# Kernel optimization log

Measured on AMD Instinct MI355X. Metric: run time of the kernel, lower is better.

Reference implementation:

```python
import jax, jax.numpy as jnp
import numpy as np

C = 768
H = 12
T = 4096
B = 1
EPS = 1e-5


def setup_inputs() -> dict:
    key = jax.random.key(0)
    ks = jax.random.split(key, 16)
    s = 0.02
    return {
        "x": jax.random.normal(ks[0], (B, T, C), jnp.float32),
        "ln1_w": jnp.ones((C,), jnp.float32),
        "ln1_b": jnp.zeros((C,), jnp.float32),
        "W_attn": jax.random.normal(ks[1], (C, 3 * C), jnp.float32) * s,
        "b_attn": jnp.zeros((3 * C,), jnp.float32),
        "W_proj": jax.random.normal(ks[2], (C, C), jnp.float32) * s,
        "b_proj": jnp.zeros((C,), jnp.float32),
        "ln2_w": jnp.ones((C,), jnp.float32),
        "ln2_b": jnp.zeros((C,), jnp.float32),
        "W_fc": jax.random.normal(ks[3], (C, 4 * C), jnp.float32) * s,
        "b_fc": jnp.zeros((4 * C,), jnp.float32),
        "W_fc2": jax.random.normal(ks[4], (4 * C, C), jnp.float32) * s,
        "b_fc2": jnp.zeros((C,), jnp.float32),
    }


def _layernorm(x, w, b):
    mu = jnp.mean(x, axis=-1, keepdims=True)
    var = jnp.var(x, axis=-1, keepdims=True)
    return (x - mu) * jax.lax.rsqrt(var + EPS) * w + b


def _attn(x, W_attn, b_attn, W_proj, b_proj):
    Bb, Tt, Cc = x.shape
    hd = Cc // H
    qkv = x @ W_attn + b_attn                       # (B,T,3C)
    q, k, v = jnp.split(qkv, 3, axis=-1)
    q = q.reshape(Bb, Tt, H, hd).transpose(0, 2, 1, 3)  # (B,H,T,hd)
    k = k.reshape(Bb, Tt, H, hd).transpose(0, 2, 1, 3)
    v = v.reshape(Bb, Tt, H, hd).transpose(0, 2, 1, 3)
    att = jnp.einsum('bhqd,bhkd->bhqk', q, k) * (1.0 / np.sqrt(hd))
    causal = jnp.tril(jnp.ones((Tt, Tt), bool))
    att = jnp.where(causal, att, -jnp.inf)
    att = jax.nn.softmax(att, axis=-1)
    y = jnp.einsum('bhqk,bhkd->bhqd', att, v)       # (B,H,T,hd)
    y = y.transpose(0, 2, 1, 3).reshape(Bb, Tt, Cc)
    return y @ W_proj + b_proj


def _mlp(x, W_fc, b_fc, W_fc2, b_fc2):
    h = jax.nn.gelu(x @ W_fc + b_fc, approximate=False)
    return h @ W_fc2 + b_fc2


def reference(x, ln1_w, ln1_b, W_attn, b_attn, W_proj, b_proj,
              ln2_w, ln2_b, W_fc, b_fc, W_fc2, b_fc2):
    x = x + _attn(_layernorm(x, ln1_w, ln1_b), W_attn, b_attn, W_proj, b_proj)
    x = x + _mlp(_layernorm(x, ln2_w, ln2_b), W_fc, b_fc, W_fc2, b_fc2)
    return x
```

## Files before the change

kernel.cpp:

```cpp
#include <hip/hip_runtime.h>
#include <hip/hip_bf16.h>
#include <math.h>

#define TSEQ 4096
#define CDIM 768
#define NH 12
#define HD 64

typedef float f32x4 __attribute__((ext_vector_type(4)));
typedef __bf16 bf16x8 __attribute__((ext_vector_type(8)));
typedef short s16x8 __attribute__((ext_vector_type(8)));
typedef uint u32x4 __attribute__((ext_vector_type(4)));

__device__ inline ushort f2bf(float f) {
  __hip_bfloat16 h = __float2bfloat16(f);
  return __builtin_bit_cast(ushort, h);
}

__device__ inline void async16(const void* g, void* l) {
  __builtin_amdgcn_global_load_lds(
      (__attribute__((address_space(1))) unsigned int*)(uintptr_t)g,
      (__attribute__((address_space(3))) unsigned int*)(uintptr_t)l, 16, 0, 0);
}

__device__ inline void barrier_all() {
  asm volatile("s_waitcnt vmcnt(0) lgkmcnt(0)" ::: "memory");
  __builtin_amdgcn_sched_barrier(0);
  __builtin_amdgcn_s_barrier();
  __builtin_amdgcn_sched_barrier(0);
}

__device__ inline float exp2_fast(float x) {
  float r;
  asm volatile("v_exp_f32 %0, %1\n\ts_nop 0" : "=v"(r) : "v"(x));
  return r;
}

__device__ inline uint cvtpk(float a, float b) {
  uint r;
  asm volatile("v_cvt_pk_bf16_f32 %0, %1, %2" : "=v"(r) : "v"(a), "v"(b));
  return r;
}

__device__ inline bf16x8 frag_read(const ushort* base, int row, int kk, int lane) {
  const int byte = row * 128 + ((((kk * 4 + (lane >> 4)) ^ (row & 7))) << 4);
  return *(const bf16x8*)((const char*)base + byte);
}

__global__ __launch_bounds__(256) void wconv_t(
    const float* __restrict__ W, ushort* __restrict__ Wt, int K, int N)
{
  __shared__ float sm[32][33];
  const int n0 = blockIdx.x * 32, k0 = blockIdx.y * 32;
  const int c = threadIdx.x & 31, r0 = threadIdx.x >> 5;
#pragma unroll
  for (int i = 0; i < 4; ++i) {
    const int r = r0 + i * 8;
    sm[r][c] = W[(size_t)(k0 + r) * N + n0 + c];
  }
  __syncthreads();
#pragma unroll
  for (int i = 0; i < 4; ++i) {
    const int r = r0 + i * 8;
    Wt[(size_t)(n0 + r) * K + k0 + c] = f2bf(sm[c][r]);
  }
}

__global__ __launch_bounds__(256) void ln_kernel(
    const float* __restrict__ x, const float* __restrict__ w,
    const float* __restrict__ b, ushort* __restrict__ out)
{
  const int row = blockIdx.x;
  const int tid = threadIdx.x;
  const float* xr = x + (size_t)row * CDIM;
  float v[3];
  float s1 = 0.f, s2 = 0.f;
#pragma unroll
  for (int i = 0; i < 3; ++i) {
    v[i] = xr[tid + i * 256];
    s1 += v[i];
    s2 += v[i] * v[i];
  }
#pragma unroll
  for (int off = 32; off >= 1; off >>= 1) {
    s1 += __shfl_xor(s1, off, 64);
    s2 += __shfl_xor(s2, off, 64);
  }
  __shared__ float red1[4], red2[4];
  if ((tid & 63) == 0) { red1[tid >> 6] = s1; red2[tid >> 6] = s2; }
  __syncthreads();
  s1 = red1[0] + red1[1] + red1[2] + red1[3];
  s2 = red2[0] + red2[1] + red2[2] + red2[3];
  const float mu = s1 * (1.f / CDIM);
  const float var = s2 * (1.f / CDIM) - mu * mu;
  const float inv = rsqrtf(var + 1e-5f);
#pragma unroll
  for (int i = 0; i < 3; ++i) {
    const int c = tid + i * 256;
    out[(size_t)row * CDIM + c] = f2bf((v[i] - mu) * inv * w[c] + b[c]);
  }
}

template <int EPI, int BN>
__global__ __launch_bounds__(256) void gemm_bt(
    const ushort* __restrict__ A, const ushort* __restrict__ Bt,
    const float* __restrict__ bias, const float* __restrict__ res,
    ushort* __restrict__ outb, float* __restrict__ outf,
    int M, int N, int K, int gx)
{
  constexpr int NW = BN / 32;
  __shared__ __align__(16) ushort As[2][128 * 32];
  __shared__ __align__(16) ushort Bs[2][BN * 32];
  const int tid = threadIdx.x;
  const int lane = tid & 63;
  const int wv = tid >> 6;
  const int nwg = (int)gridDim.x;
  const int bid = (int)blockIdx.x;
  const int sw = (bid & 7) * (nwg >> 3) + (bid >> 3);
  const int rowBase = (sw / gx) * 128;
  const int colBase = (sw % gx) * BN;
  const int wr = (wv >> 1) * 64;
  const int wc = (wv & 1) * (BN / 2);

  f32x4 acc[4][NW] = {};

  const int e0 = tid * 8;
  const int r0 = e0 >> 5, c0 = e0 & 31;
  const int e1 = (tid + 256) * 8;
  const int r1 = e1 >> 5, c1 = e1 & 31;

  const ushort* Ag0 = A + (size_t)(rowBase + r0) * K + c0;
  const ushort* Ag1 = A + (size_t)(rowBase + r1) * K + c1;
  const ushort* Bg0 = Bt + (size_t)(colBase + r0) * K + c0;
  const ushort* Bg1 = Bt + (size_t)(colBase + r1) * K + c1;

  auto stage = [&](int buf, int k0) {
    async16(Ag0 + k0, &As[buf][e0]);
    async16(Ag1 + k0, &As[buf][e1]);
    async16(Bg0 + k0, &Bs[buf][e0]);
    if (BN == 128) async16(Bg1 + k0, &Bs[buf][e1]);
  };

  stage(0, 0);
  int buf = 0;
  for (int k0 = 0; k0 < K; k0 += 32) {
    barrier_all();
    if (k0 + 32 < K) stage(buf ^ 1, k0 + 32);
    bf16x8 af[4], bfr[NW];
#pragma unroll
    for (int m = 0; m < 4; ++m)
      af[m] = *(const bf16x8*)&As[buf][(wr + m * 16 + (lane & 15)) * 32 + (lane >> 4) * 8];
#pragma unroll
    for (int n = 0; n < NW; ++n)
      bfr[n] = *(const bf16x8*)&Bs[buf][(wc + n * 16 + (lane & 15)) * 32 + (lane >> 4) * 8];
#pragma unroll
    for (int m = 0; m < 4; ++m)
#pragma unroll
      for (int n = 0; n < NW; ++n)
        acc[m][n] = __builtin_amdgcn_mfma_f32_16x16x32_bf16(af[m], bfr[n], acc[m][n], 0, 0, 0);
    buf ^= 1;
  }

#pragma unroll
  for (int n = 0; n < NW; ++n) {
    const int gc = colBase + wc + n * 16 + (lane & 15);
    const float bv = bias[gc];
#pragma unroll
    for (int m = 0; m < 4; ++m) {
#pragma unroll
      for (int j = 0; j < 4; ++j) {
        const int gr = rowBase + wr + m * 16 + (lane >> 4) * 4 + j;
        const float v = acc[m][n][j] + bv;
        if (EPI == 0) {
          outb[(size_t)gr * N + gc] = f2bf(v);
        } else if (EPI == 1) {
          outf[(size_t)gr * N + gc] = res[(size_t)gr * N + gc] + v;
        } else {
          const float g = 0.5f * v * (1.0f + erff(v * 0.70710678118654752f));
          outb[(size_t)gr * N + gc] = f2bf(g);
        }
      }
    }
  }
}

__global__ __launch_bounds__(256) void attn_kernel(
    const ushort* __restrict__ qkv, ushort* __restrict__ att)
{
  __shared__ __align__(16) ushort Ks[2][64 * 64];
  __shared__ __align__(16) ushort Vt[2][64 * 64];

  const int tid = threadIdx.x;
  const int lane = tid & 63;
  const int wv = tid >> 6;
  const int g = lane >> 4;
  const int ql = lane & 15;
  const int p_ = blockIdx.x & 255, grp = blockIdx.x >> 8;
  const int item = (grp & 1) ? (grp * 256 + 255 - p_) : (grp * 256 + p_);
  const int qb = 63 - (item / 12);
  const int h = item % 12;
  const int t0 = qb * 64;
  const size_t rs = 3 * CDIM;
  const int qo = h * HD, ko = CDIM + h * HD, vo = 2 * CDIM + h * HD;

  const float cexp = 0.18033688f;
  const float cbias = -32.0f * 0.18033688f;

  const int L0 = tid * 16, L1 = (tid + 256) * 16;
  const int r_0 = L0 >> 7, c_0 = ((L0 >> 4) & 7) ^ (r_0 & 7);
  const int r_1 = L1 >> 7, c_1 = ((L1 >> 4) & 7) ^ (r_1 & 7);
  const ushort* kg0 = qkv + (size_t)r_0 * rs + ko + c_0 * 8;
  const ushort* kg1 = qkv + (size_t)r_1 * rs + ko + c_1 * 8;

  const int vt = (tid >> 3) * 2;
  const int vd = (tid & 7) * 8;
  const int slot2 = (32 * ((vt >> 4) >> 1) + 8 * ((vt >> 2) & 3) +
                     4 * ((vt >> 4) & 1) + (vt & 3)) * 2;
  const ushort* vg = qkv + (size_t)vt * rs + vo + vd;

  const ushort* qrow = qkv + (size_t)(t0 + wv * 16 + ql) * rs + qo + g * 8;
  const bf16x8 aq0 = *(const bf16x8*)(qrow);
  const bf16x8 aq1 = *(const bf16x8*)(qrow + 32);

  s16x8 vA0 = *(const s16x8*)(vg);
  s16x8 vA1 = *(const s16x8*)(vg + rs);
  async16(kg0, (char*)Ks[0] + L0);
  async16(kg1, (char*)Ks[0] + L1);
  asm volatile("s_waitcnt vmcnt(0)" ::: "memory");
#pragma unroll
  for (int jj = 0; jj < 8; ++jj) {
    const int d = vd + jj;
    const uint val = (uint)(ushort)vA0[jj] | ((uint)(ushort)vA1[jj] << 16);
    *(uint*)((char*)Vt[0] + d * 128 + (slot2 ^ (((d >> 1) & 7) << 4))) = val;
  }

  float lsum = 0.f;
  f32x4 accO[4] = {};
  const int swzv = (ql >> 1) & 7;

  auto body = [&](int kb, int cur, bool diag) {
    barrier_all();

    s16x8 vN0, vN1;
    const bool pre = (kb < qb);
    if (pre) {
      const size_t koff = (size_t)(kb + 1) * 64 * rs;
      vN0 = *(const s16x8*)(vg + koff);
      vN1 = *(const s16x8*)(vg + koff + rs);
      async16(kg0 + koff, (char*)Ks[cur ^ 1] + L0);
      async16(kg1 + koff, (char*)Ks[cur ^ 1] + L1);
    }

    f32x4 accS[4] = {};
    __builtin_amdgcn_s_setprio(1);
#pragma unroll
    for (int kk = 0; kk < 2; ++kk) {
      const bf16x8 a_q = kk ? aq1 : aq0;
#pragma unroll
      for (int n = 0; n < 4; ++n)
        accS[n] = __builtin_amdgcn_mfma_f32_16x16x32_bf16(
            frag_read(Ks[cur], n * 16 + ql, kk, lane), a_q, accS[n], 0, 0, 0);
    }
    __builtin_amdgcn_s_setprio(0);

    uint pk[8];
#pragma unroll
    for (int n = 0; n < 4; ++n) {
      float pv[4];
#pragma unroll
      for (int j = 0; j < 4; ++j) {
        float s = exp2_fast(fmaf(accS[n][j], cexp, cbias));
        if (diag && (kb * 64 + 16 * n + 4 * g + j) > (t0 + wv * 16 + ql)) s = 0.f;
        pv[j] = s;
        lsum += s;
      }
      pk[2 * n] = cvtpk(pv[0], pv[1]);
      pk[2 * n + 1] = cvtpk(pv[2], pv[3]);
    }
    const bf16x8 pf0 = __builtin_bit_cast(bf16x8, (u32x4){pk[0], pk[1], pk[2], pk[3]});
    const bf16x8 pf1 = __builtin_bit_cast(bf16x8, (u32x4){pk[4], pk[5], pk[6], pk[7]});

    __builtin_amdgcn_s_setprio(1);
#pragma unroll
    for (int kk = 0; kk < 2; ++kk) {
      const bf16x8 a_p = kk ? pf1 : pf0;
#pragma unroll
      for (int n = 0; n < 4; ++n) {
        const int byte = (n * 16 + ql) * 128 + ((kk * 64 + g * 16) ^ (swzv << 4));
        const bf16x8 bv = *(const bf16x8*)((const char*)Vt[cur] + byte);
        accO[n] = __builtin_amdgcn_mfma_f32_16x16x32_bf16(a_p, bv, accO[n], 0, 0, 0);
      }
    }
    __builtin_amdgcn_s_setprio(0);

    if (pre) {
#pragma unroll
      for (int jj = 0; jj < 8; ++jj) {
        const int d = vd + jj;
        const uint val = (uint)(ushort)vN0[jj] | ((uint)(ushort)vN1[jj] << 16);
        *(uint*)((char*)Vt[cur ^ 1] + d * 128 + (slot2 ^ (((d >> 1) & 7) << 4))) = val;
      }
    }
  };

  int cur = 0;
  for (int kb = 0; kb < qb; ++kb) {
    body(kb, cur, false);
    cur ^= 1;
  }
  body(qb, cur, true);

  lsum += __shfl_xor(lsum, 16, 64);
  lsum += __shfl_xor(lsum, 32, 64);
  float inv[4];
#pragma unroll
  for (int jr = 0; jr < 4; ++jr)
    inv[jr] = 1.0f / __shfl(lsum, 4 * g + jr, 64);
#pragma unroll
  for (int n = 0; n < 4; ++n)
#pragma unroll
    for (int jr = 0; jr < 4; ++jr) {
      const int tq = t0 + wv * 16 + 4 * g + jr;
      const int d = n * 16 + ql;
      att[(size_t)tq * CDIM + h * HD + d] = f2bf(accO[n][jr] * inv[jr]);
    }
}

extern "C" void kernel_launch(void* const* d_in, const int* in_sizes, int n_in,
                              void* d_out, int out_size, void* d_ws, size_t ws_size,
                              hipStream_t stream)
{
  const float* x      = (const float*)d_in[0];
  const float* ln1_w  = (const float*)d_in[1];
  const float* ln1_b  = (const float*)d_in[2];
  const float* W_attn = (const float*)d_in[3];
  const float* b_attn = (const float*)d_in[4];
  const float* W_proj = (const float*)d_in[5];
  const float* b_proj = (const float*)d_in[6];
  const float* ln2_w  = (const float*)d_in[7];
  const float* ln2_b  = (const float*)d_in[8];
  const float* W_fc   = (const float*)d_in[9];
  const float* b_fc   = (const float*)d_in[10];
  const float* W_fc2  = (const float*)d_in[11];
  const float* b_fc2  = (const float*)d_in[12];
  float* out = (float*)d_out;

  char* base = (char*)d_ws;
  size_t off = 0;
  auto alloc = [&](size_t bytes) -> void* {
    void* q = base + off;
    off = (off + bytes + 255) & ~(size_t)255;
    return q;
  };
  ushort* Wt_attn = (ushort*)alloc(768ull * 2304 * 2);
  ushort* Wt_proj = (ushort*)alloc(768ull * 768 * 2);
  ushort* Wt_fc   = (ushort*)alloc(768ull * 3072 * 2);
  ushort* Wt_fc2  = (ushort*)alloc(3072ull * 768 * 2);
  ushort* t_ln    = (ushort*)alloc(4096ull * 768 * 2);
  ushort* t_att   = (ushort*)alloc(4096ull * 768 * 2);
  float*  t_x1    = (float*) alloc(4096ull * 768 * 4);
  ushort* t_big   = (ushort*)alloc(4096ull * 3072 * 2);
  ushort* t_qkv = t_big;
  ushort* t_h   = t_big;

  wconv_t<<<dim3(2304 / 32, 768 / 32), 256, 0, stream>>>(W_attn, Wt_attn, 768, 2304);
  wconv_t<<<dim3(768 / 32, 768 / 32), 256, 0, stream>>>(W_proj, Wt_proj, 768, 768);
  wconv_t<<<dim3(3072 / 32, 768 / 32), 256, 0, stream>>>(W_fc, Wt_fc, 768, 3072);
  wconv_t<<<dim3(768 / 32, 3072 / 32), 256, 0, stream>>>(W_fc2, Wt_fc2, 3072, 768);

  ln_kernel<<<4096, 256, 0, stream>>>(x, ln1_w, ln1_b, t_ln);
  gemm_bt<0, 128><<<18 * 32, 256, 0, stream>>>(
      t_ln, Wt_attn, b_attn, nullptr, t_qkv, nullptr, 4096, 2304, 768, 18);
  attn_kernel<<<dim3(768), 256, 0, stream>>>(t_qkv, t_att);
  gemm_bt<1, 64><<<12 * 32, 256, 0, stream>>>(
      t_att, Wt_proj, b_proj, x, nullptr, t_x1, 4096, 768, 768, 12);
  ln_kernel<<<4096, 256, 0, stream>>>(t_x1, ln2_w, ln2_b, t_ln);
  gemm_bt<2, 128><<<24 * 32, 256, 0, stream>>>(
      t_ln, Wt_fc, b_fc, nullptr, t_h, nullptr, 4096, 3072, 768, 24);
  gemm_bt<1, 64><<<12 * 32, 256, 0, stream>>>(
      t_h, Wt_fc2, b_fc2, t_x1, nullptr, out, 4096, 768, 3072, 12);
}
```

Measured before the change: 202.2 us.

## Split attention KV range across waves with per-wave staging and LDS reduction

Restructures the attention kernel so each of the four waves handles all 64 queries of the block but a strided quarter of the key/value blocks, using its own private K/V LDS buffers. Inter-wave barriers disappear from the main loop, and each K/V fragment read from LDS is reused across four query groups. The row sum is computed with an MFMA against a vector of ones instead of scalar adds, and the partial outputs are combined through a 96KB LDS reduction at the end. In exchange it uses far more LDS and registers (launch bounds force one block per SM slot), adds an epilogue reduction, and can leave waves unevenly loaded on short causal rows.

```diff
diff --git a/kernel.cpp b/kernel.cpp
--- a/kernel.cpp
+++ b/kernel.cpp
@@ -184,146 +184,189 @@
   }
 }
 
-__global__ __launch_bounds__(256) void attn_kernel(
+__global__ __launch_bounds__(256, 1) void attn_kernel(
     const ushort* __restrict__ qkv, ushort* __restrict__ att)
 {
-  __shared__ __align__(16) ushort Ks[2][64 * 64];
-  __shared__ __align__(16) ushort Vt[2][64 * 64];
-
+  __shared__ __align__(16) char smem[98304];
   const int tid = threadIdx.x;
   const int lane = tid & 63;
   const int wv = tid >> 6;
-  const int g = lane >> 4;
+  const int g = (lane >> 4) & 3;
   const int ql = lane & 15;
   const int p_ = blockIdx.x & 255, grp = blockIdx.x >> 8;
   const int item = (grp & 1) ? (grp * 256 + 255 - p_) : (grp * 256 + p_);
-  const int qb = 63 - (item / 12);
+  const int qb = 63 - item / 12;
   const int h = item % 12;
   const int t0 = qb * 64;
-  const size_t rs = 3 * CDIM;
+  const int rs = 3 * CDIM;
   const int qo = h * HD, ko = CDIM + h * HD, vo = 2 * CDIM + h * HD;
 
   const float cexp = 0.18033688f;
   const float cbias = -32.0f * 0.18033688f;
 
-  const int L0 = tid * 16, L1 = (tid + 256) * 16;
-  const int r_0 = L0 >> 7, c_0 = ((L0 >> 4) & 7) ^ (r_0 & 7);
-  const int r_1 = L1 >> 7, c_1 = ((L1 >> 4) & 7) ^ (r_1 & 7);
-  const ushort* kg0 = qkv + (size_t)r_0 * rs + ko + c_0 * 8;
-  const ushort* kg1 = qkv + (size_t)r_1 * rs + ko + c_1 * 8;
-
-  const int vt = (tid >> 3) * 2;
-  const int vd = (tid & 7) * 8;
-  const int slot2 = (32 * ((vt >> 4) >> 1) + 8 * ((vt >> 2) & 3) +
-                     4 * ((vt >> 4) & 1) + (vt & 3)) * 2;
-  const ushort* vg = qkv + (size_t)vt * rs + vo + vd;
-
-  const ushort* qrow = qkv + (size_t)(t0 + wv * 16 + ql) * rs + qo + g * 8;
-  const bf16x8 aq0 = *(const bf16x8*)(qrow);
-  const bf16x8 aq1 = *(const bf16x8*)(qrow + 32);
-
-  s16x8 vA0 = *(const s16x8*)(vg);
-  s16x8 vA1 = *(const s16x8*)(vg + rs);
-  async16(kg0, (char*)Ks[0] + L0);
-  async16(kg1, (char*)Ks[0] + L1);
-  asm volatile("s_waitcnt vmcnt(0)" ::: "memory");
-#pragma unroll
-  for (int jj = 0; jj < 8; ++jj) {
-    const int d = vd + jj;
-    const uint val = (uint)(ushort)vA0[jj] | ((uint)(ushort)vA1[jj] << 16);
-    *(uint*)((char*)Vt[0] + d * 128 + (slot2 ^ (((d >> 1) & 7) << 4))) = val;
-  }
-
-  float lsum = 0.f;
-  f32x4 accO[4] = {};
-  const int swzv = (ql >> 1) & 7;
-
-  auto body = [&](int kb, int cur, bool diag) {
-    barrier_all();
-
-    s16x8 vN0, vN1;
-    const bool pre = (kb < qb);
-    if (pre) {
-      const size_t koff = (size_t)(kb + 1) * 64 * rs;
-      vN0 = *(const s16x8*)(vg + koff);
-      vN1 = *(const s16x8*)(vg + koff + rs);
-      async16(kg0 + koff, (char*)Ks[cur ^ 1] + L0);
-      async16(kg1 + koff, (char*)Ks[cur ^ 1] + L1);
-    }
-
-    f32x4 accS[4] = {};
-    __builtin_amdgcn_s_setprio(1);
-#pragma unroll
-    for (int kk = 0; kk < 2; ++kk) {
-      const bf16x8 a_q = kk ? aq1 : aq0;
-#pragma unroll
-      for (int n = 0; n < 4; ++n)
-        accS[n] = __builtin_amdgcn_mfma_f32_16x16x32_bf16(
-            frag_read(Ks[cur], n * 16 + ql, kk, lane), a_q, accS[n], 0, 0, 0);
-    }
-    __builtin_amdgcn_s_setprio(0);
-
-    uint pk[8];
-#pragma unroll
-    for (int n = 0; n < 4; ++n) {
-      float pv[4];
-#pragma unroll
-      for (int j = 0; j < 4; ++j) {
-        float s = exp2_fast(fmaf(accS[n][j], cexp, cbias));
-        if (diag && (kb * 64 + 16 * n + 4 * g + j) > (t0 + wv * 16 + ql)) s = 0.f;
-        pv[j] = s;
-        lsum += s;
-      }
-      pk[2 * n] = cvtpk(pv[0], pv[1]);
-      pk[2 * n + 1] = cvtpk(pv[2], pv[3]);
-    }
-    const bf16x8 pf0 = __builtin_bit_cast(bf16x8, (u32x4){pk[0], pk[1], pk[2], pk[3]});
-    const bf16x8 pf1 = __builtin_bit_cast(bf16x8, (u32x4){pk[4], pk[5], pk[6], pk[7]});
-
-    __builtin_amdgcn_s_setprio(1);
-#pragma unroll
-    for (int kk = 0; kk < 2; ++kk) {
-      const bf16x8 a_p = kk ? pf1 : pf0;
-#pragma unroll
-      for (int n = 0; n < 4; ++n) {
-        const int byte = (n * 16 + ql) * 128 + ((kk * 64 + g * 16) ^ (swzv << 4));
-        const bf16x8 bv = *(const bf16x8*)((const char*)Vt[cur] + byte);
-        accO[n] = __builtin_amdgcn_mfma_f32_16x16x32_bf16(a_p, bv, accO[n], 0, 0, 0);
-      }
-    }
-    __builtin_amdgcn_s_setprio(0);
-
-    if (pre) {
+  char* wbase = smem + wv * 24576;
+  char* vtile = wbase + 16384;
+
+  bf16x8 qf[4][2];
+#pragma unroll
+  for (int qg = 0; qg < 4; ++qg) {
+    const ushort* qrow = qkv + (size_t)(t0 + 16 * qg + ql) * rs + qo + g * 8;
+    qf[qg][0] = *(const bf16x8*)(qrow);
+    qf[qg][1] = *(const bf16x8*)(qrow + 32);
+  }
+
+  const int krow = lane >> 3;
+  const ushort* bKsrc = qkv + (size_t)(wv * 64 + krow) * rs + ko + ((lane & 7) ^ krow) * 8;
+
+  const int vt2 = (lane >> 3) * 2;
+  const int vd = (lane & 7) * 8;
+  const ushort* bVsrc = qkv + (size_t)(wv * 64 + vt2) * rs + vo + vd;
+  int slot2[4];
+#pragma unroll
+  for (int i = 0; i < 4; ++i)
+    slot2[i] = (32 * (i >> 1) + 8 * (vt2 >> 2) + 4 * (i & 1) + (vt2 & 3)) * 2;
+
+  const int nt = (qb >= wv) ? ((qb - wv) >> 2) + 1 : 0;
+
+  auto stageK = [&](int buf, size_t koff) {
+    char* dK = wbase + buf * 8192;
+#pragma unroll
+    for (int i = 0; i < 8; ++i)
+      async16(bKsrc + koff + (size_t)i * 8 * rs, dK + i * 1024 + lane * 16);
+  };
+
+  s16x8 vr[4][2];
+  if (nt > 0) {
+    stageK(0, 0);
+#pragma unroll
+    for (int i = 0; i < 4; ++i) {
+      vr[i][0] = *(const s16x8*)(bVsrc + (size_t)i * 16 * rs);
+      vr[i][1] = *(const s16x8*)(bVsrc + (size_t)i * 16 * rs + rs);
+    }
+  }
+
+  f32x4 accO[4][4] = {};
+  f32x4 accL[4] = {};
+  const bf16x8 ones = __builtin_bit_cast(bf16x8,
+      (u32x4){0x3F803F80u, 0x3F803F80u, 0x3F803F80u, 0x3F803F80u});
+
+  int kv0 = wv * 64;
+  int cur = 0;
+  for (int it = 0; it < nt; ++it) {
+    asm volatile("s_waitcnt vmcnt(0)" ::: "memory");
+    __builtin_amdgcn_sched_barrier(0);
+    const size_t nextoff = (size_t)(it + 1) * 256 * rs;
+    const bool pre = (it + 1 < nt);
+    if (pre) stageK(cur ^ 1, nextoff);
+
+#pragma unroll
+    for (int i = 0; i < 4; ++i) {
 #pragma unroll
       for (int jj = 0; jj < 8; ++jj) {
         const int d = vd + jj;
-        const uint val = (uint)(ushort)vN0[jj] | ((uint)(ushort)vN1[jj] << 16);
-        *(uint*)((char*)Vt[cur ^ 1] + d * 128 + (slot2 ^ (((d >> 1) & 7) << 4))) = val;
-      }
-    }
-  };
-
-  int cur = 0;
-  for (int kb = 0; kb < qb; ++kb) {
-    body(kb, cur, false);
+        const uint val = (uint)(ushort)vr[i][0][jj] | ((uint)(ushort)vr[i][1][jj] << 16);
+        *(uint*)(vtile + d * 128 + (slot2[i] ^ (((d >> 1) & 7) << 4))) = val;
+      }
+    }
+    if (pre) {
+#pragma unroll
+      for (int i = 0; i < 4; ++i) {
+        vr[i][0] = *(const s16x8*)(bVsrc + nextoff + (size_t)i * 16 * rs);
+        vr[i][1] = *(const s16x8*)(bVsrc + nextoff + (size_t)i * 16 * rs + rs);
+      }
+    }
+
+    const ushort* Kt = (const ushort*)(wbase + cur * 8192);
+    const bool diag = (kv0 == t0);
+    uint paw[4][8];
+#pragma unroll
+    for (int kg = 0; kg < 4; ++kg) {
+      const bf16x8 A0 = frag_read(Kt, kg * 16 + ql, 0, lane);
+      const bf16x8 A1 = frag_read(Kt, kg * 16 + ql, 1, lane);
+      f32x4 s[4];
+#pragma unroll
+      for (int qg = 0; qg < 4; ++qg) {
+        s[qg] = __builtin_amdgcn_mfma_f32_16x16x32_bf16(A0, qf[qg][0], (f32x4){0.f, 0.f, 0.f, 0.f}, 0, 0, 0);
+        s[qg] = __builtin_amdgcn_mfma_f32_16x16x32_bf16(A1, qf[qg][1], s[qg], 0, 0, 0);
+      }
+#pragma unroll
+      for (int qg = 0; qg < 4; ++qg) {
+        float e[4];
+#pragma unroll
+        for (int j = 0; j < 4; ++j) {
+          float p = exp2_fast(fmaf(s[qg][j], cexp, cbias));
+          if (diag && (kv0 + kg * 16 + 4 * g + j) > (t0 + 16 * qg + ql)) p = 0.f;
+          e[j] = p;
+        }
+        paw[qg][(kg >> 1) * 4 + (kg & 1) * 2]     = cvtpk(e[0], e[1]);
+        paw[qg][(kg >> 1) * 4 + (kg & 1) * 2 + 1] = cvtpk(e[2], e[3]);
+      }
+    }
+    bf16x8 pa[4][2];
+#pragma unroll
+    for (int qg = 0; qg < 4; ++qg) {
+      pa[qg][0] = __builtin_bit_cast(bf16x8, (u32x4){paw[qg][0], paw[qg][1], paw[qg][2], paw[qg][3]});
+      pa[qg][1] = __builtin_bit_cast(bf16x8, (u32x4){paw[qg][4], paw[qg][5], paw[qg][6], paw[qg][7]});
+    }
+
+    asm volatile("s_waitcnt lgkmcnt(0)" ::: "memory");
+    __builtin_amdgcn_sched_barrier(0);
+
+#pragma unroll
+    for (int dg = 0; dg < 4; ++dg) {
+#pragma unroll
+      for (int kk = 0; kk < 2; ++kk) {
+        const int byte = (16 * dg + ql) * 128 + ((kk * 64 + g * 16) ^ (((ql >> 1) & 7) << 4));
+        const bf16x8 bv = *(const bf16x8*)(vtile + byte);
+#pragma unroll
+        for (int qg = 0; qg < 4; ++qg)
+          accO[qg][dg] = __builtin_amdgcn_mfma_f32_16x16x32_bf16(pa[qg][kk], bv, accO[qg][dg], 0, 0, 0);
+      }
+    }
+#pragma unroll
+    for (int qg = 0; qg < 4; ++qg) {
+      accL[qg] = __builtin_amdgcn_mfma_f32_16x16x32_bf16(pa[qg][0], ones, accL[qg], 0, 0, 0);
+      accL[qg] = __builtin_amdgcn_mfma_f32_16x16x32_bf16(pa[qg][1], ones, accL[qg], 0, 0, 0);
+    }
+    kv0 += 256;
     cur ^= 1;
   }
-  body(qb, cur, true);
-
-  lsum += __shfl_xor(lsum, 16, 64);
-  lsum += __shfl_xor(lsum, 32, 64);
-  float inv[4];
-#pragma unroll
-  for (int jr = 0; jr < 4; ++jr)
-    inv[jr] = 1.0f / __shfl(lsum, 4 * g + jr, 64);
-#pragma unroll
-  for (int n = 0; n < 4; ++n)
-#pragma unroll
-    for (int jr = 0; jr < 4; ++jr) {
-      const int tq = t0 + wv * 16 + 4 * g + jr;
-      const int d = n * 16 + ql;
-      att[(size_t)tq * CDIM + h * HD + d] = f2bf(accO[n][jr] * inv[jr]);
-    }
+
+  __syncthreads();
+  float* smO = (float*)smem;
+  float* smL = (float*)(smem + 65536);
+#pragma unroll
+  for (int qg = 0; qg < 4; ++qg)
+#pragma unroll
+    for (int dg = 0; dg < 4; ++dg) {
+      const int d = 16 * dg + ql;
+      *(f32x4*)&smO[(size_t)(wv * 64 + d) * 64 + ((16 * qg + 4 * g) ^ ((d & 7) << 2))] = accO[qg][dg];
+    }
+  if (ql == 0) {
+#pragma unroll
+    for (int qg = 0; qg < 4; ++qg)
+      *(f32x4*)&smL[wv * 64 + 16 * qg + 4 * g] = accL[qg];
+  }
+  __syncthreads();
+
+  const int q0 = 16 * wv + 4 * g;
+  f32x4 ls = {0.f, 0.f, 0.f, 0.f};
+#pragma unroll
+  for (int w2 = 0; w2 < 4; ++w2) ls += *(const f32x4*)&smL[w2 * 64 + q0];
+  f32x4 inv;
+#pragma unroll
+  for (int j = 0; j < 4; ++j) inv[j] = 1.0f / ls[j];
+#pragma unroll
+  for (int n = 0; n < 4; ++n) {
+    const int d = 16 * n + ql;
+    f32x4 o = {0.f, 0.f, 0.f, 0.f};
+#pragma unroll
+    for (int w2 = 0; w2 < 4; ++w2)
+      o += *(const f32x4*)&smO[(size_t)(w2 * 64 + d) * 64 + (q0 ^ ((d & 7) << 2))];
+#pragma unroll
+    for (int j = 0; j < 4; ++j)
+      att[(size_t)(t0 + q0 + j) * CDIM + h * HD + d] = f2bf(o[j] * inv[j]);
+  }
 }
 
 extern "C" void kernel_launch(void* const* d_in, const int* in_sizes, int n_in,
```

Result: slower. 222.7 us (+10.2%).

## Triple-buffer GEMM k-loop with partial vmcnt waits and loosen attention waits

Applied to the files above, without the earlier changes.

The GEMM main loop moves from double to triple buffering in LDS, prefetching two tiles ahead and waiting only on the older tile's loads via vmcnt counts instead of draining all loads. MFMA issue gets raised wave priority. The attention loop is turned from a lambda into a single loop that issues the next V global loads before the barrier and waits with vmcnt(2), so those loads overlap the current block's work. The aim is to hide global-load latency behind compute, at the cost of more LDS use and hand-counted vmcnt values that must match the number of outstanding loads exactly.

```diff
diff --git a/kernel.cpp b/kernel.cpp
--- a/kernel.cpp
+++ b/kernel.cpp
@@ -21,13 +21,6 @@
   __builtin_amdgcn_global_load_lds(
       (__attribute__((address_space(1))) unsigned int*)(uintptr_t)g,
       (__attribute__((address_space(3))) unsigned int*)(uintptr_t)l, 16, 0, 0);
-}
-
-__device__ inline void barrier_all() {
-  asm volatile("s_waitcnt vmcnt(0) lgkmcnt(0)" ::: "memory");
-  __builtin_amdgcn_sched_barrier(0);
-  __builtin_amdgcn_s_barrier();
-  __builtin_amdgcn_sched_barrier(0);
 }
 
 __device__ inline float exp2_fast(float x) {
@@ -109,8 +102,8 @@
     int M, int N, int K, int gx)
 {
   constexpr int NW = BN / 32;
-  __shared__ __align__(16) ushort As[2][128 * 32];
-  __shared__ __align__(16) ushort Bs[2][BN * 32];
+  __shared__ __align__(16) ushort As[3][128 * 32];
+  __shared__ __align__(16) ushort Bs[3][BN * 32];
   const int tid = threadIdx.x;
   const int lane = tid & 63;
   const int wv = tid >> 6;
@@ -141,24 +134,37 @@
     if (BN == 128) async16(Bg1 + k0, &Bs[buf][e1]);
   };
 
+  const int nt = K / 32;
   stage(0, 0);
-  int buf = 0;
-  for (int k0 = 0; k0 < K; k0 += 32) {
-    barrier_all();
-    if (k0 + 32 < K) stage(buf ^ 1, k0 + 32);
+  stage(1, 32);
+  int b0 = 0, b1 = 1, b2 = 2;
+  for (int t = 0; t < nt; ++t) {
+    if (t < nt - 1) {
+      if (BN == 128) asm volatile("s_waitcnt vmcnt(4)" ::: "memory");
+      else           asm volatile("s_waitcnt vmcnt(3)" ::: "memory");
+    } else {
+      asm volatile("s_waitcnt vmcnt(0)" ::: "memory");
+    }
+    __builtin_amdgcn_sched_barrier(0);
+    __builtin_amdgcn_s_barrier();
+    __builtin_amdgcn_sched_barrier(0);
+    if (t + 2 < nt) stage(b2, t * 32 + 64);
+
     bf16x8 af[4], bfr[NW];
 #pragma unroll
     for (int m = 0; m < 4; ++m)
-      af[m] = *(const bf16x8*)&As[buf][(wr + m * 16 + (lane & 15)) * 32 + (lane >> 4) * 8];
+      af[m] = *(const bf16x8*)&As[b0][(wr + m * 16 + (lane & 15)) * 32 + (lane >> 4) * 8];
 #pragma unroll
     for (int n = 0; n < NW; ++n)
-      bfr[n] = *(const bf16x8*)&Bs[buf][(wc + n * 16 + (lane & 15)) * 32 + (lane >> 4) * 8];
+      bfr[n] = *(const bf16x8*)&Bs[b0][(wc + n * 16 + (lane & 15)) * 32 + (lane >> 4) * 8];
+    __builtin_amdgcn_s_setprio(1);
 #pragma unroll
     for (int m = 0; m < 4; ++m)
 #pragma unroll
       for (int n = 0; n < NW; ++n)
         acc[m][n] = __builtin_amdgcn_mfma_f32_16x16x32_bf16(af[m], bfr[n], acc[m][n], 0, 0, 0);
-    buf ^= 1;
+    __builtin_amdgcn_s_setprio(0);
+    const int tmp = b0; b0 = b1; b1 = b2; b2 = tmp;
   }
 
 #pragma unroll
@@ -226,7 +232,6 @@
   s16x8 vA1 = *(const s16x8*)(vg + rs);
   async16(kg0, (char*)Ks[0] + L0);
   async16(kg1, (char*)Ks[0] + L1);
-  asm volatile("s_waitcnt vmcnt(0)" ::: "memory");
 #pragma unroll
   for (int jj = 0; jj < 8; ++jj) {
     const int d = vd + jj;
@@ -238,15 +243,23 @@
   f32x4 accO[4] = {};
   const int swzv = (ql >> 1) & 7;
 
-  auto body = [&](int kb, int cur, bool diag) {
-    barrier_all();
-
-    s16x8 vN0, vN1;
+  int cur = 0;
+  for (int kb = 0; kb <= qb; ++kb) {
     const bool pre = (kb < qb);
+    const bool diag = (kb == qb);
+    const size_t koff = (size_t)(kb + 1) * 64 * rs;
+
     if (pre) {
-      const size_t koff = (size_t)(kb + 1) * 64 * rs;
-      vN0 = *(const s16x8*)(vg + koff);
-      vN1 = *(const s16x8*)(vg + koff + rs);
+      vA0 = *(const s16x8*)(vg + koff);
+      vA1 = *(const s16x8*)(vg + koff + rs);
+    }
+    if (pre) asm volatile("s_waitcnt vmcnt(2) lgkmcnt(0)" ::: "memory");
+    else     asm volatile("s_waitcnt vmcnt(0) lgkmcnt(0)" ::: "memory");
+    __builtin_amdgcn_sched_barrier(0);
+    __builtin_amdgcn_s_barrier();
+    __builtin_amdgcn_sched_barrier(0);
+
+    if (pre) {
       async16(kg0 + koff, (char*)Ks[cur ^ 1] + L0);
       async16(kg1 + koff, (char*)Ks[cur ^ 1] + L1);
     }
@@ -297,18 +310,12 @@
 #pragma unroll
       for (int jj = 0; jj < 8; ++jj) {
         const int d = vd + jj;
-        const uint val = (uint)(ushort)vN0[jj] | ((uint)(ushort)vN1[jj] << 16);
+        const uint val = (uint)(ushort)vA0[jj] | ((uint)(ushort)vA1[jj] << 16);
         *(uint*)((char*)Vt[cur ^ 1] + d * 128 + (slot2 ^ (((d >> 1) & 7) << 4))) = val;
       }
     }
-  };
-
-  int cur = 0;
-  for (int kb = 0; kb < qb; ++kb) {
-    body(kb, cur, false);
     cur ^= 1;
   }
-  body(qb, cur, true);
 
   lsum += __shfl_xor(lsum, 16, 64);
   lsum += __shfl_xor(lsum, 32, 64);
```

New measurement: 205.1 us. Within noise of the previous version (+1.4%).
